# Kernel optimization log

Measured on AMD Instinct MI355X. Metric: run time of the kernel, lower is better.

## Reference

```python
import jax, jax.numpy as jnp
import numpy as np

EMB = 768
HS = 64
B, T = 4, 4096


def setup_inputs() -> dict:
    key = jax.random.key(0)
    ks = jax.random.split(key, 7)
    s = 1.0 / np.sqrt(EMB)
    return {
        "x": jax.random.normal(ks[0], (B, T, EMB), dtype=jnp.float32),
        "Wk": jax.random.normal(ks[1], (EMB, HS), dtype=jnp.float32) * s,
        "bk": jnp.zeros((HS,), dtype=jnp.float32),
        "Wq": jax.random.normal(ks[2], (EMB, HS), dtype=jnp.float32) * s,
        "bq": jnp.zeros((HS,), dtype=jnp.float32),
        "Wv": jax.random.normal(ks[3], (EMB, HS), dtype=jnp.float32) * s,
        "bv": jnp.zeros((HS,), dtype=jnp.float32),
    }


def reference(x, Wk, bk, Wq, bq, Wv, bv):
    # Linear projections: (B, T, emb) @ (emb, hs) + bias -> (B, T, hs)
    k = x @ Wk + bk
    q = x @ Wq + bq
    v = x @ Wv + bv
    # NOTE: original code computes key @ query^T (k on the left), no 1/sqrt(hs) scaling.
    att = jnp.einsum("bth,bsh->bts", k, q)  # (B, T, T)
    causal = jnp.tril(jnp.ones((T, T), dtype=bool))  # (T, T)
    att = jnp.where(causal, att, -jnp.inf)
    wei = jax.nn.softmax(att, axis=-1)
    return jnp.einsum("bts,bsh->bth", wei, v)  # (B, T, hs)
```

## Files before the change

kernel.cpp:

```cpp
#include <hip/hip_runtime.h>
#include <cmath>

static constexpr int EMB  = 768;
static constexpr int HS   = 64;
static constexpr int NB   = 4;
static constexpr int SEQ  = 4096;
static constexpr int MTOT = NB * SEQ;
static constexpr int SPLITS = 8;

typedef __attribute__((ext_vector_type(8))) short  short8x;
typedef __attribute__((ext_vector_type(4))) float  float4x;
typedef __attribute__((ext_vector_type(4))) unsigned short ushort4x;

__device__ inline unsigned short rne16(float f) {
    unsigned u = __builtin_bit_cast(unsigned, f);
    unsigned r = u + 0x7FFFu + ((u >> 16) & 1u);
    return (unsigned short)(r >> 16);
}
__device__ inline float bf2f(unsigned short h) {
    return __builtin_bit_cast(float, ((unsigned)h) << 16);
}

__global__ __launch_bounds__(256) void convert_w(
    const float* __restrict__ Wk, const float* __restrict__ Wq, const float* __restrict__ Wv,
    unsigned short* __restrict__ wpk)
{
    const int t    = blockIdx.x * 256 + threadIdx.x;
    const int lane = t & 63;
    const int rest = t >> 6;
    const int nng  = rest % 12;
    const int kcp  = rest / 12;
    const int kc   = kcp % 24;
    const int p    = kcp / 24;
    const int which= nng >> 2;
    const int nn   = nng & 3;
    const float* W = (which == 0) ? Wk : (which == 1) ? Wq : Wv;
    const int col  = nn * 16 + (lane & 15);
    const int kr   = kc * 32 + (lane >> 4) * 8;

    unsigned short o[8];
    #pragma unroll
    for (int j = 0; j < 8; ++j) {
        float w = W[(size_t)(kr + j) * HS + col];
        unsigned short h = rne16(w);
        o[j] = (p == 0) ? h : rne16(w - bf2f(h));
    }
    size_t base = ((size_t)((p * 24 + kc) * 12 + nng) * 64 + lane) * 8;
    *(short8x*)&wpk[base] = *(short8x*)o;
}

__global__ __launch_bounds__(256) void proj_kernel(
    const float* __restrict__ x,
    const unsigned short* __restrict__ wpk,
    const float* __restrict__ bk, const float* __restrict__ bq, const float* __restrict__ bv,
    unsigned short* __restrict__ khi, unsigned short* __restrict__ klo,
    unsigned short* __restrict__ qhi, unsigned short* __restrict__ qlo,
    unsigned short* __restrict__ vT)
{
    __shared__ unsigned short xh[2][32 * 72];
    __shared__ unsigned short xl[2][32 * 72];

    const int tid  = threadIdx.x;
    const int lane = tid & 63;
    const int w    = tid >> 6;
    const int l15  = lane & 15;
    const int quad = lane >> 4;
    const int row0 = blockIdx.x * 32;

    float4x acc[3][2] = {};
    float4  pre[2];

    #pragma unroll
    for (int it = 0; it < 2; ++it) {
        const int fi = tid + it * 256;
        const int r  = fi >> 4, c4 = (fi & 15) * 4;
        pre[it] = *(const float4*)&x[(size_t)(row0 + r) * EMB + 0 * 64 + c4];
    }
    #pragma unroll
    for (int it = 0; it < 2; ++it) {
        const int fi = tid + it * 256;
        const int r  = fi >> 4, c4 = (fi & 15) * 4;
        const float4 xv = pre[it];
        const unsigned short h0 = rne16(xv.x), h1 = rne16(xv.y),
                             h2 = rne16(xv.z), h3 = rne16(xv.w);
        ushort4x hv = {h0, h1, h2, h3};
        ushort4x lv = {rne16(xv.x - bf2f(h0)), rne16(xv.y - bf2f(h1)),
                       rne16(xv.z - bf2f(h2)), rne16(xv.w - bf2f(h3))};
        *(ushort4x*)&xh[0][r * 72 + c4] = hv;
        *(ushort4x*)&xl[0][r * 72 + c4] = lv;
    }

    for (int ch = 0; ch < 12; ++ch) {
        if (ch + 1 < 12) {
            #pragma unroll
            for (int it = 0; it < 2; ++it) {
                const int fi = tid + it * 256;
                const int r  = fi >> 4, c4 = (fi & 15) * 4;
                pre[it] = *(const float4*)&x[(size_t)(row0 + r) * EMB + (ch + 1) * 64 + c4];
            }
        }
        __syncthreads();
        const int buf = ch & 1;

        #pragma unroll
        for (int k0i = 0; k0i < 2; ++k0i) {
            const int k0 = k0i * 32;
            const int kc = ch * 2 + k0i;
            short8x ah[2], al[2];
            #pragma unroll
            for (int mi = 0; mi < 2; ++mi) {
                ah[mi] = *(const short8x*)&xh[buf][(mi * 16 + l15) * 72 + k0 + quad * 8];
                al[mi] = *(const short8x*)&xl[buf][(mi * 16 + l15) * 72 + k0 + quad * 8];
            }
            #pragma unroll
            for (int which = 0; which < 3; ++which) {
                const int nng = which * 4 + w;
                const short8x bh = *(const short8x*)&wpk[((size_t)((0 * 24 + kc) * 12 + nng) * 64 + lane) * 8];
                const short8x bl = *(const short8x*)&wpk[((size_t)((1 * 24 + kc) * 12 + nng) * 64 + lane) * 8];
                #pragma unroll
                for (int mi = 0; mi < 2; ++mi) {
                    acc[which][mi] = __builtin_amdgcn_mfma_f32_16x16x32_bf16(ah[mi], bh, acc[which][mi], 0, 0, 0);
                    acc[which][mi] = __builtin_amdgcn_mfma_f32_16x16x32_bf16(ah[mi], bl, acc[which][mi], 0, 0, 0);
                    acc[which][mi] = __builtin_amdgcn_mfma_f32_16x16x32_bf16(al[mi], bh, acc[which][mi], 0, 0, 0);
                }
            }
        }

        if (ch + 1 < 12) {
            const int nbuf = (ch + 1) & 1;
            #pragma unroll
            for (int it = 0; it < 2; ++it) {
                const int fi = tid + it * 256;
                const int r  = fi >> 4, c4 = (fi & 15) * 4;
                const float4 xv = pre[it];
                const unsigned short h0 = rne16(xv.x), h1 = rne16(xv.y),
                                     h2 = rne16(xv.z), h3 = rne16(xv.w);
                ushort4x hv = {h0, h1, h2, h3};
                ushort4x lv = {rne16(xv.x - bf2f(h0)), rne16(xv.y - bf2f(h1)),
                               rne16(xv.z - bf2f(h2)), rne16(xv.w - bf2f(h3))};
                *(ushort4x*)&xh[nbuf][r * 72 + c4] = hv;
                *(ushort4x*)&xl[nbuf][r * 72 + c4] = lv;
            }
        }
    }

    const int col = w * 16 + l15;
    const float bkv = bk[col], bqv = bq[col], bvv = bv[col];
    #pragma unroll
    for (int mi = 0; mi < 2; ++mi) {
        const int rbase = row0 + mi * 16 + quad * 4;
        #pragma unroll
        for (int r = 0; r < 4; ++r) {
            const float kv = acc[0][mi][r] + bkv;
            const unsigned short hk = rne16(kv);
            khi[(size_t)(rbase + r) * 64 + col] = hk;
            klo[(size_t)(rbase + r) * 64 + col] = rne16(kv - bf2f(hk));
            const float qv = acc[1][mi][r] + bqv;
            const unsigned short hq = rne16(qv);
            qhi[(size_t)(rbase + r) * 64 + col] = hq;
            qlo[(size_t)(rbase + r) * 64 + col] = rne16(qv - bf2f(hq));
        }
        const int b = rbase / SEQ;
        const int s = rbase % SEQ;
        ushort4x vv = {rne16(acc[2][mi][0] + bvv), rne16(acc[2][mi][1] + bvv),
                       rne16(acc[2][mi][2] + bvv), rne16(acc[2][mi][3] + bvv)};
        *(ushort4x*)&vT[((size_t)b * 64 + col) * SEQ + s] = vv;
    }
}

__global__ __launch_bounds__(256, 2) void attn_kernel(
    const unsigned short* __restrict__ khi, const unsigned short* __restrict__ klo,
    const unsigned short* __restrict__ qhi, const unsigned short* __restrict__ qlo,
    const unsigned short* __restrict__ vT,
    float* __restrict__ Opart, float* __restrict__ lpart)
{
    __shared__ unsigned short qh_s[64 * 72];
    __shared__ unsigned short ql_s[64 * 72];
    __shared__ unsigned short vt_s[64 * 72];
    __shared__ unsigned short psH[64 * 72];
    __shared__ unsigned short psL[64 * 72];

    const int tid  = threadIdx.x;
    const int lane = tid & 63;
    const int w    = tid >> 6;
    const int l15  = lane & 15;
    const int quad = lane >> 4;

    const int n  = blockIdx.x;
    const int sp = n & (SPLITS - 1);
    const int b  = (n >> 3) & (NB - 1);
    const int p  = n >> 5;
    const int jj[4] = {63 - p, 32 + p, 31 - p, p};
    const size_t rowb = (size_t)b * SEQ;

    float4x oacc[4][4] = {};
    float   l_r[4][4]  = {};

    const int sr = tid >> 3;
    const int c8 = (tid & 7) * 8;

    short8x pq[2], pl[2], pv[2];
    {
        const int s0 = sp * 64;
        #pragma unroll
        for (int it = 0; it < 2; ++it) {
            const int r = sr + it * 32;
            pq[it] = *(const short8x*)&qhi[(rowb + s0 + r) * 64 + c8];
            pl[it] = *(const short8x*)&qlo[(rowb + s0 + r) * 64 + c8];
            pv[it] = *(const short8x*)&vT[((size_t)b * 64 + r) * SEQ + s0 + c8];
        }
    }

    for (int ci = sp; ci <= jj[0]; ci += SPLITS) {
        const int s0 = ci * 64;

        short8x ah[4][2], al[4][2];
        bool av[4];
        #pragma unroll
        for (int idx = 0; idx < 4; ++idx) {
            av[idx] = (ci <= jj[idx]);
            if (av[idx]) {
                #pragma unroll
                for (int k0 = 0; k0 < 2; ++k0) {
                    const size_t rr = (rowb + jj[idx] * 64 + 16 * w + l15) * 64 + k0 * 32 + quad * 8;
                    ah[idx][k0] = *(const short8x*)&khi[rr];
                    al[idx][k0] = *(const short8x*)&klo[rr];
                }
            }
        }

        __syncthreads();
        #pragma unroll
        for (int it = 0; it < 2; ++it) {
            const int r = sr + it * 32;
            *(short8x*)&qh_s[r * 72 + c8] = pq[it];
            *(short8x*)&ql_s[r * 72 + c8] = pl[it];
            *(short8x*)&vt_s[r * 72 + c8] = pv[it];
        }
        if (ci + SPLITS <= jj[0]) {
            const int s1 = (ci + SPLITS) * 64;
            #pragma unroll
            for (int it = 0; it < 2; ++it) {
                const int r = sr + it * 32;
                pq[it] = *(const short8x*)&qhi[(rowb + s1 + r) * 64 + c8];
                pl[it] = *(const short8x*)&qlo[(rowb + s1 + r) * 64 + c8];
                pv[it] = *(const short8x*)&vT[((size_t)b * 64 + r) * SEQ + s1 + c8];
            }
        }
        __syncthreads();

        #pragma unroll
        for (int g = 0; g < 2; ++g) {
            const int idxH = g ? 1 : 0;
            const int idxL = g ? 2 : 3;
            const int jH = jj[idxH], jL = jj[idxL];
            const bool aH = av[idxH], aL = av[idxL];
            if (!aH && !aL) continue;

            float4x sH[4] = {}, sL[4] = {};
            __builtin_amdgcn_s_setprio(1);
            #pragma unroll
            for (int k0 = 0; k0 < 2; ++k0) {
                #pragma unroll
                for (int nn = 0; nn < 4; ++nn) {
                    const short8x bh = *(const short8x*)&qh_s[(nn * 16 + l15) * 72 + k0 * 32 + quad * 8];
                    const short8x bl = *(const short8x*)&ql_s[(nn * 16 + l15) * 72 + k0 * 32 + quad * 8];
                    if (aH) {
                        sH[nn] = __builtin_amdgcn_mfma_f32_16x16x32_bf16(ah[idxH][k0], bh, sH[nn], 0, 0, 0);
                        sH[nn] = __builtin_amdgcn_mfma_f32_16x16x32_bf16(al[idxH][k0], bh, sH[nn], 0, 0, 0);
                        sH[nn] = __builtin_amdgcn_mfma_f32_16x16x32_bf16(ah[idxH][k0], bl, sH[nn], 0, 0, 0);
                    }
                    if (aL) {
                        sL[nn] = __builtin_amdgcn_mfma_f32_16x16x32_bf16(ah[idxL][k0], bh, sL[nn], 0, 0, 0);
                        sL[nn] = __builtin_amdgcn_mfma_f32_16x16x32_bf16(al[idxL][k0], bh, sL[nn], 0, 0, 0);
                        sL[nn] = __builtin_amdgcn_mfma_f32_16x16x32_bf16(ah[idxL][k0], bl, sL[nn], 0, 0, 0);
                    }
                }
            }
            __builtin_amdgcn_s_setprio(0);

            #pragma unroll
            for (int hl = 0; hl < 2; ++hl) {
                const bool alive = hl ? aL : aH;
                if (!alive) continue;
                const int j   = hl ? jL : jH;
                const int idx = hl ? idxL : idxH;
                float4x* sc   = hl ? sL : sH;
                unsigned short* ps = hl ? psL : psH;
                if (ci == j) {
                    const int trow = j * 64 + 16 * w + quad * 4;
                    #pragma unroll
                    for (int nn = 0; nn < 4; ++nn) {
                        const int colg = s0 + nn * 16 + l15;
                        #pragma unroll
                        for (int r = 0; r < 4; ++r)
                            if (colg > trow + r) sc[nn][r] = -1e30f;
                    }
                }
                #pragma unroll
                for (int nn = 0; nn < 4; ++nn) {
                    #pragma unroll
                    for (int r = 0; r < 4; ++r) {
                        const float e = __expf(fminf(sc[nn][r], 80.0f));
                        const unsigned short h = rne16(e);
                        l_r[idx][r] += bf2f(h);
                        ps[(16 * w + quad * 4 + r) * 72 + nn * 16 + l15] = h;
                    }
                }
            }

            __builtin_amdgcn_s_setprio(1);
            #pragma unroll
            for (int k0 = 0; k0 < 2; ++k0) {
                short8x paH, paL;
                if (aH) paH = *(const short8x*)&psH[(16 * w + l15) * 72 + k0 * 32 + quad * 8];
                if (aL) paL = *(const short8x*)&psL[(16 * w + l15) * 72 + k0 * 32 + quad * 8];
                #pragma unroll
                for (int nn = 0; nn < 4; ++nn) {
                    const short8x vb = *(const short8x*)&vt_s[(nn * 16 + l15) * 72 + k0 * 32 + quad * 8];
                    if (aH) oacc[idxH][nn] = __builtin_amdgcn_mfma_f32_16x16x32_bf16(paH, vb, oacc[idxH][nn], 0, 0, 0);
                    if (aL) oacc[idxL][nn] = __builtin_amdgcn_mfma_f32_16x16x32_bf16(paL, vb, oacc[idxL][nn], 0, 0, 0);
                }
            }
            __builtin_amdgcn_s_setprio(0);
        }
    }

    #pragma unroll
    for (int idx = 0; idx < 4; ++idx) {
        const int j = jj[idx];
        if (idx == 3 && sp > p) continue;
        float lv[4];
        #pragma unroll
        for (int r = 0; r < 4; ++r) {
            float l = l_r[idx][r];
            l += __shfl_xor(l, 1);
            l += __shfl_xor(l, 2);
            l += __shfl_xor(l, 4);
            l += __shfl_xor(l, 8);
            lv[r] = l;
        }
        const size_t part = (size_t)(j * NB + b) * SPLITS + sp;
        float* Op = Opart + part * 4096;
        #pragma unroll
        for (int nn = 0; nn < 4; ++nn)
            #pragma unroll
            for (int r = 0; r < 4; ++r)
                Op[(16 * w + quad * 4 + r) * 64 + nn * 16 + l15] = oacc[idx][nn][r];
        if (l15 == 0) {
            #pragma unroll
            for (int r = 0; r < 4; ++r)
                lpart[part * 64 + 16 * w + quad * 4 + r] = lv[r];
        }
    }
}

__global__ __launch_bounds__(256) void combine_kernel(
    const float* __restrict__ Opart, const float* __restrict__ lpart,
    float* __restrict__ out)
{
    const int j   = blockIdx.x;
    const int b   = blockIdx.y;
    const int tid = threadIdx.x;
    const int row = blockIdx.z * 16 + (tid >> 4);
    const int c0  = (tid & 15) * 4;
    const size_t base = (size_t)(j * NB + b) * SPLITS;

    float4 acc = {0.f, 0.f, 0.f, 0.f};
    float lsum = 0.f;
    for (int sp = 0; sp < SPLITS; ++sp) {
        const float l = lpart[(base + sp) * 64 + row];
        if (l > 0.f) {
            lsum += l;
            const float4 v = *(const float4*)&Opart[(base + sp) * 4096 + row * 64 + c0];
            acc.x += v.x; acc.y += v.y; acc.z += v.z; acc.w += v.w;
        }
    }
    const float inv = 1.0f / lsum;
    float4 v;
    v.x = acc.x * inv; v.y = acc.y * inv; v.z = acc.z * inv; v.w = acc.w * inv;
    *(float4*)&out[((size_t)b * SEQ + j * 64 + row) * 64 + c0] = v;
}

extern "C" void kernel_launch(void* const* d_in, const int* in_sizes, int n_in,
                              void* d_out, int out_size, void* d_ws, size_t ws_size,
                              hipStream_t stream)
{
    const float* x  = (const float*)d_in[0];
    const float* Wk = (const float*)d_in[1];
    const float* bk = (const float*)d_in[2];
    const float* Wq = (const float*)d_in[3];
    const float* bq = (const float*)d_in[4];
    const float* Wv = (const float*)d_in[5];
    const float* bv = (const float*)d_in[6];
    float* out = (float*)d_out;

    const size_t NE = (size_t)MTOT * HS;
    unsigned short* khi = (unsigned short*)d_ws;
    unsigned short* klo = khi + NE;
    unsigned short* qhi = klo + NE;
    unsigned short* qlo = qhi + NE;
    unsigned short* vT  = qlo + NE;
    unsigned short* wpk = vT + NE;
    float* Opart = (float*)(wpk + 294912);
    float* lpart = Opart + (size_t)64 * NB * SPLITS * 4096;

    hipMemsetAsync(lpart, 0, (size_t)64 * NB * SPLITS * 64 * sizeof(float), stream);
    convert_w<<<144, 256, 0, stream>>>(Wk, Wq, Wv, wpk);
    proj_kernel<<<MTOT / 32, 256, 0, stream>>>(x, wpk, bk, bq, bv, khi, klo, qhi, qlo, vT);
    attn_kernel<<<16 * NB * SPLITS, 256, 0, stream>>>(khi, klo, qhi, qlo, vT, Opart, lpart);
    dim3 cgrid(64, NB, 4);
    combine_kernel<<<cgrid, 256, 0, stream>>>(Opart, lpart, out);
}
```

Baseline: 176.4 us.

## Double-buffer Q/V shared tiles and load K fragments per group

Shared-memory Q-hi, Q-lo and V tiles are now double-buffered. The next tile is written into the alternate buffer while the current one is consumed, so each iteration needs one barrier instead of two. K fragments are loaded per group just before use rather than for all four row blocks up front, which is meant to cut register pressure. In exchange, LDS usage grows, which may lower occupancy, and the K global loads now sit closer to their MFMA consumers, leaving less latency to hide.

```diff
diff --git a/kernel.cpp b/kernel.cpp
--- a/kernel.cpp
+++ b/kernel.cpp
@@ -174,9 +174,9 @@
     const unsigned short* __restrict__ vT,
     float* __restrict__ Opart, float* __restrict__ lpart)
 {
-    __shared__ unsigned short qh_s[64 * 72];
-    __shared__ unsigned short ql_s[64 * 72];
-    __shared__ unsigned short vt_s[64 * 72];
+    __shared__ unsigned short qh_s[2][64 * 72];
+    __shared__ unsigned short ql_s[2][64 * 72];
+    __shared__ unsigned short vt_s[2][64 * 72];
     __shared__ unsigned short psH[64 * 72];
     __shared__ unsigned short psL[64 * 72];
 
@@ -209,36 +209,15 @@
             pl[it] = *(const short8x*)&qlo[(rowb + s0 + r) * 64 + c8];
             pv[it] = *(const short8x*)&vT[((size_t)b * 64 + r) * SEQ + s0 + c8];
         }
-    }
-
-    for (int ci = sp; ci <= jj[0]; ci += SPLITS) {
-        const int s0 = ci * 64;
-
-        short8x ah[4][2], al[4][2];
-        bool av[4];
-        #pragma unroll
-        for (int idx = 0; idx < 4; ++idx) {
-            av[idx] = (ci <= jj[idx]);
-            if (av[idx]) {
-                #pragma unroll
-                for (int k0 = 0; k0 < 2; ++k0) {
-                    const size_t rr = (rowb + jj[idx] * 64 + 16 * w + l15) * 64 + k0 * 32 + quad * 8;
-                    ah[idx][k0] = *(const short8x*)&khi[rr];
-                    al[idx][k0] = *(const short8x*)&klo[rr];
-                }
-            }
-        }
-
-        __syncthreads();
         #pragma unroll
         for (int it = 0; it < 2; ++it) {
             const int r = sr + it * 32;
-            *(short8x*)&qh_s[r * 72 + c8] = pq[it];
-            *(short8x*)&ql_s[r * 72 + c8] = pl[it];
-            *(short8x*)&vt_s[r * 72 + c8] = pv[it];
-        }
-        if (ci + SPLITS <= jj[0]) {
-            const int s1 = (ci + SPLITS) * 64;
+            *(short8x*)&qh_s[0][r * 72 + c8] = pq[it];
+            *(short8x*)&ql_s[0][r * 72 + c8] = pl[it];
+            *(short8x*)&vt_s[0][r * 72 + c8] = pv[it];
+        }
+        if (sp + SPLITS <= jj[0]) {
+            const int s1 = (sp + SPLITS) * 64;
             #pragma unroll
             for (int it = 0; it < 2; ++it) {
                 const int r = sr + it * 32;
@@ -247,15 +226,59 @@
                 pv[it] = *(const short8x*)&vT[((size_t)b * 64 + r) * SEQ + s1 + c8];
             }
         }
-        __syncthreads();
+    }
+    __syncthreads();
+
+    int cur = 0;
+    for (int ci = sp; ci <= jj[0]; ci += SPLITS) {
+        const int s0 = ci * 64;
+
+        if (ci + SPLITS <= jj[0]) {
+            #pragma unroll
+            for (int it = 0; it < 2; ++it) {
+                const int r = sr + it * 32;
+                *(short8x*)&qh_s[cur ^ 1][r * 72 + c8] = pq[it];
+                *(short8x*)&ql_s[cur ^ 1][r * 72 + c8] = pl[it];
+                *(short8x*)&vt_s[cur ^ 1][r * 72 + c8] = pv[it];
+            }
+            if (ci + 2 * SPLITS <= jj[0]) {
+                const int s2 = (ci + 2 * SPLITS) * 64;
+                #pragma unroll
+                for (int it = 0; it < 2; ++it) {
+                    const int r = sr + it * 32;
+                    pq[it] = *(const short8x*)&qhi[(rowb + s2 + r) * 64 + c8];
+                    pl[it] = *(const short8x*)&qlo[(rowb + s2 + r) * 64 + c8];
+                    pv[it] = *(const short8x*)&vT[((size_t)b * 64 + r) * SEQ + s2 + c8];
+                }
+            }
+        }
+
+        const unsigned short* qhc = qh_s[cur];
+        const unsigned short* qlc = ql_s[cur];
+        const unsigned short* vtc = vt_s[cur];
 
         #pragma unroll
         for (int g = 0; g < 2; ++g) {
             const int idxH = g ? 1 : 0;
             const int idxL = g ? 2 : 3;
             const int jH = jj[idxH], jL = jj[idxL];
-            const bool aH = av[idxH], aL = av[idxL];
+            const bool aH = (ci <= jH), aL = (ci <= jL);
             if (!aH && !aL) continue;
+
+            short8x ahH[2], alH[2], ahL[2], alL[2];
+            #pragma unroll
+            for (int k0 = 0; k0 < 2; ++k0) {
+                if (aH) {
+                    const size_t rH = (rowb + jH * 64 + 16 * w + l15) * 64 + k0 * 32 + quad * 8;
+                    ahH[k0] = *(const short8x*)&khi[rH];
+                    alH[k0] = *(const short8x*)&klo[rH];
+                }
+                if (aL) {
+                    const size_t rL = (rowb + jL * 64 + 16 * w + l15) * 64 + k0 * 32 + quad * 8;
+                    ahL[k0] = *(const short8x*)&khi[rL];
+                    alL[k0] = *(const short8x*)&klo[rL];
+                }
+            }
 
             float4x sH[4] = {}, sL[4] = {};
             __builtin_amdgcn_s_setprio(1);
@@ -263,17 +286,17 @@
             for (int k0 = 0; k0 < 2; ++k0) {
                 #pragma unroll
                 for (int nn = 0; nn < 4; ++nn) {
-                    const short8x bh = *(const short8x*)&qh_s[(nn * 16 + l15) * 72 + k0 * 32 + quad * 8];
-                    const short8x bl = *(const short8x*)&ql_s[(nn * 16 + l15) * 72 + k0 * 32 + quad * 8];
+                    const short8x bh = *(const short8x*)&qhc[(nn * 16 + l15) * 72 + k0 * 32 + quad * 8];
+                    const short8x bl = *(const short8x*)&qlc[(nn * 16 + l15) * 72 + k0 * 32 + quad * 8];
                     if (aH) {
-                        sH[nn] = __builtin_amdgcn_mfma_f32_16x16x32_bf16(ah[idxH][k0], bh, sH[nn], 0, 0, 0);
-                        sH[nn] = __builtin_amdgcn_mfma_f32_16x16x32_bf16(al[idxH][k0], bh, sH[nn], 0, 0, 0);
-                        sH[nn] = __builtin_amdgcn_mfma_f32_16x16x32_bf16(ah[idxH][k0], bl, sH[nn], 0, 0, 0);
+                        sH[nn] = __builtin_amdgcn_mfma_f32_16x16x32_bf16(ahH[k0], bh, sH[nn], 0, 0, 0);
+                        sH[nn] = __builtin_amdgcn_mfma_f32_16x16x32_bf16(alH[k0], bh, sH[nn], 0, 0, 0);
+                        sH[nn] = __builtin_amdgcn_mfma_f32_16x16x32_bf16(ahH[k0], bl, sH[nn], 0, 0, 0);
                     }
                     if (aL) {
-                        sL[nn] = __builtin_amdgcn_mfma_f32_16x16x32_bf16(ah[idxL][k0], bh, sL[nn], 0, 0, 0);
-                        sL[nn] = __builtin_amdgcn_mfma_f32_16x16x32_bf16(al[idxL][k0], bh, sL[nn], 0, 0, 0);
-                        sL[nn] = __builtin_amdgcn_mfma_f32_16x16x32_bf16(ah[idxL][k0], bl, sL[nn], 0, 0, 0);
+                        sL[nn] = __builtin_amdgcn_mfma_f32_16x16x32_bf16(ahL[k0], bh, sL[nn], 0, 0, 0);
+                        sL[nn] = __builtin_amdgcn_mfma_f32_16x16x32_bf16(alL[k0], bh, sL[nn], 0, 0, 0);
+                        sL[nn] = __builtin_amdgcn_mfma_f32_16x16x32_bf16(ahL[k0], bl, sL[nn], 0, 0, 0);
                     }
                 }
             }
@@ -317,13 +340,16 @@
                 if (aL) paL = *(const short8x*)&psL[(16 * w + l15) * 72 + k0 * 32 + quad * 8];
                 #pragma unroll
                 for (int nn = 0; nn < 4; ++nn) {
-                    const short8x vb = *(const short8x*)&vt_s[(nn * 16 + l15) * 72 + k0 * 32 + quad * 8];
+                    const short8x vb = *(const short8x*)&vtc[(nn * 16 + l15) * 72 + k0 * 32 + quad * 8];
                     if (aH) oacc[idxH][nn] = __builtin_amdgcn_mfma_f32_16x16x32_bf16(paH, vb, oacc[idxH][nn], 0, 0, 0);
                     if (aL) oacc[idxL][nn] = __builtin_amdgcn_mfma_f32_16x16x32_bf16(paL, vb, oacc[idxL][nn], 0, 0, 0);
                 }
             }
             __builtin_amdgcn_s_setprio(0);
         }
+
+        __syncthreads();
+        cur ^= 1;
     }
 
     #pragma unroll
```

After: 167.8 us. -4.9%, faster.
